# Kernel tuning notes

Measured on AMD Instinct MI355X. Metric: run time of the kernel, lower is better.

Reference implementation:

```python
import jax, jax.numpy as jnp
import numpy as np

PRUNE_N, PRUNE_M = 2, 4
RIA_A = 1.0
NUM_HEADS = 16
HEAD_DIM = 128
ROPE_THETA = 10000.0


def sparse_mask(W, scaler_row, perm):
    # RIA metric: |W|/colsum + |W|/rowsum, scaled by sqrt(scaler_row)**a
    absW = jnp.abs(W)
    metric = (absW / absW.sum(axis=0, keepdims=True)
              + absW / absW.sum(axis=1, keepdims=True))
    metric = metric * (jnp.sqrt(scaler_row)[None, :] ** RIA_A)
    Wm = metric @ perm                      # permute columns: [R, C]
    R, C = Wm.shape
    nb = C // PRUNE_M
    blocks = Wm.reshape(R, nb, PRUNE_M)
    # hard N:M mask: top-n per block of m
    _, idx = jax.lax.top_k(blocks, PRUNE_N)           # [R, nb, n]
    hard = jax.nn.one_hot(idx, PRUNE_M, dtype=Wm.dtype).sum(axis=-2)  # [R, nb, m]
    soft = jax.nn.softmax(blocks, axis=-1)
    hard = hard.reshape(R, C) @ perm.T
    soft = soft.reshape(R, C) @ perm.T
    # straight-through estimator
    return jax.lax.stop_gradient(hard - soft) + soft


def sparse_linear(x, W, b, scaler_row, perm):
    Wm = W * sparse_mask(W, scaler_row, perm)
    y = jnp.einsum('bsh,oh->bso', x, Wm)
    return y + b if b is not None else y


def rotate_half(x):
    x1, x2 = jnp.split(x, 2, axis=-1)
    return jnp.concatenate([-x2, x1], axis=-1)


def rope_tables(seq_len, dim, dtype):
    inv_freq = 1.0 / (ROPE_THETA ** (jnp.arange(0, dim, 2, dtype=jnp.float32) / dim))
    t = jnp.arange(seq_len, dtype=jnp.float32)
    freqs = jnp.outer(t, inv_freq)               # [S, dim/2]
    emb = jnp.concatenate([freqs, freqs], axis=-1)  # [S, dim]
    return jnp.cos(emb).astype(dtype), jnp.sin(emb).astype(dtype)


def setup_inputs() -> dict:
    key = jax.random.key(0)
    ks = jax.random.split(key, 16)
    H = 2048
    B, S = 2, 2048
    inp = {
        'hidden_states': jax.random.normal(ks[0], (B, S, H), jnp.float32) * 0.02,
        'Wq': jax.random.normal(ks[1], (H, H), jnp.float32) * 0.02,
        'bq': jax.random.normal(ks[2], (H,), jnp.float32) * 0.02,
        'Wk': jax.random.normal(ks[3], (H, H), jnp.float32) * 0.02,
        'bk': jax.random.normal(ks[4], (H,), jnp.float32) * 0.02,
        'Wv': jax.random.normal(ks[5], (H, H), jnp.float32) * 0.02,
        'bv': jax.random.normal(ks[6], (H,), jnp.float32) * 0.02,
        'Wo': jax.random.normal(ks[7], (H, H), jnp.float32) * 0.02,
        'sq': jax.random.uniform(ks[8], (H,), jnp.float32, 0.1, 1.0),
        'sk': jax.random.uniform(ks[9], (H,), jnp.float32, 0.1, 1.0),
        'sv': jax.random.uniform(ks[10], (H,), jnp.float32, 0.1, 1.0),
        'so': jax.random.uniform(ks[11], (H,), jnp.float32, 0.1, 1.0),
        'perm_qkv': jax.random.normal(ks[12], (H, H), jnp.float32) * 0.02,
        'perm_o': jax.random.normal(ks[13], (H, H), jnp.float32) * 0.02,
        'position_ids': jnp.broadcast_to(jnp.arange(S, dtype=jnp.int64), (B, S)),
    }
    return inp


def reference(hidden_states, Wq, bq, Wk, bk, Wv, bv, Wo,
              sq, sk, sv, so, perm_qkv, perm_o, position_ids):
    B, S, H = hidden_states.shape
    q = sparse_linear(hidden_states, Wq, bq, sq, perm_qkv)
    k = sparse_linear(hidden_states, Wk, bk, sk, perm_qkv)
    v = sparse_linear(hidden_states, Wv, bv, sv, perm_qkv)

    q = q.reshape(B, S, NUM_HEADS, HEAD_DIM).transpose(0, 2, 1, 3)  # [B,Hh,S,D]
    k = k.reshape(B, S, NUM_HEADS, HEAD_DIM).transpose(0, 2, 1, 3)
    v = v.reshape(B, S, NUM_HEADS, HEAD_DIM).transpose(0, 2, 1, 3)

    cos, sin = rope_tables(S, HEAD_DIM, q.dtype)
    c = cos[position_ids][:, None]  # [B,1,S,D]
    s = sin[position_ids][:, None]
    q = q * c + rotate_half(q) * s
    k = k * c + rotate_half(k) * s

    scores = jnp.einsum('bhqd,bhkd->bhqk', q, k) / np.sqrt(HEAD_DIM)
    causal = jnp.tril(jnp.ones((S, S), dtype=bool))
    scores = jnp.where(causal[None, None], scores, jnp.finfo(jnp.float32).min)
    attn = jax.nn.softmax(scores.astype(jnp.float32), axis=-1).astype(q.dtype)
    out = jnp.einsum('bhqk,bhkd->bhqd', attn, v)
    out = out.transpose(0, 2, 1, 3).reshape(B, S, H)
    out = sparse_linear(out, Wo, None, so, perm_o)
    return out
```

## Files before the change

### kernel.cpp

```cpp
#include <hip/hip_runtime.h>
#include <cstdint>
#include <cstddef>

typedef __attribute__((ext_vector_type(4))) float  f32x4;
typedef __attribute__((ext_vector_type(4))) int    i32x4;
typedef __attribute__((ext_vector_type(8))) short  s16x8;
typedef __attribute__((ext_vector_type(4))) short  s16x4;
typedef __attribute__((ext_vector_type(8))) __bf16 bf16x8;

struct Ptr4 { const float* p[4]; };

#define DEV __device__ __forceinline__

DEV unsigned short f2bf_u(float x) {
  unsigned u = __builtin_bit_cast(unsigned, x);
  u += 0x7fffu + ((u >> 16) & 1u);
  return (unsigned short)(u >> 16);
}
DEV float bfu2f(unsigned short u) {
  return __builtin_bit_cast(float, ((unsigned)u) << 16);
}
DEV bf16x8 ld_frag(const unsigned short* p) {
  s16x8 v = *(const s16x8*)p;
  return __builtin_bit_cast(bf16x8, v);
}
DEV f32x4 mfma16(bf16x8 a, bf16x8 b, f32x4 c) {
  return __builtin_amdgcn_mfma_f32_16x16x32_bf16(a, b, c, 0, 0, 0);
}
DEV void gload_lds16(const unsigned short* g, unsigned short* l) {
  __builtin_amdgcn_global_load_lds(
      (const __attribute__((address_space(1))) unsigned int*)g,
      (__attribute__((address_space(3))) unsigned int*)l, 16, 0, 0);
}
DEV int xcd_swizzle(int bid, int nwg) {
  const int q8 = nwg >> 3;
  return (bid & 7) * q8 + (bid >> 3);
}

__global__ __launch_bounds__(256)
void k_rowsum(Ptr4 Ws, float* __restrict__ rowsums)
{
  const int row = blockIdx.x, mat = blockIdx.y, tid = threadIdx.x;
  const float* W = Ws.p[mat] + (size_t)row * 2048;
  float s = 0.f;
  #pragma unroll
  for (int p = 0; p < 2; ++p) {
    f32x4 v = *(const f32x4*)(W + p * 1024 + tid * 4);
    s += fabsf(v[0]) + fabsf(v[1]) + fabsf(v[2]) + fabsf(v[3]);
  }
  #pragma unroll
  for (int off = 1; off < 64; off <<= 1) s += __shfl_xor(s, off);
  __shared__ float red[4];
  if ((tid & 63) == 0) red[tid >> 6] = s;
  __syncthreads();
  if (tid == 0) rowsums[mat * 2048 + row] = red[0] + red[1] + red[2] + red[3];
}

__global__ __launch_bounds__(256)
void k_colsum_part(Ptr4 Ws, float* __restrict__ part)
{
  const int c = blockIdx.x * 256 + threadIdx.x;
  const int r0 = blockIdx.y * 64;
  const int mat = blockIdx.z;
  const float* W = Ws.p[mat];
  float s = 0.f;
  for (int rr = 0; rr < 64; ++rr) s += fabsf(W[(size_t)(r0 + rr) * 2048 + c]);
  part[((size_t)mat * 32 + blockIdx.y) * 2048 + c] = s;
}
__global__ __launch_bounds__(256)
void k_colsum_red(const float* __restrict__ part, float* __restrict__ colsums)
{
  const int gid = blockIdx.x * 256 + threadIdx.x;
  const int mat = gid >> 11, c = gid & 2047;
  float s = 0.f;
  #pragma unroll
  for (int j = 0; j < 32; ++j) s += part[((size_t)mat * 32 + j) * 2048 + c];
  colsums[gid] = s;
}

__global__ __launch_bounds__(256)
void k_metric(Ptr4 Ws, Ptr4 Ss, const float* __restrict__ rowsums,
              const float* __restrict__ colsums,
              unsigned short* __restrict__ mhi, unsigned short* __restrict__ mlo)
{
  const size_t idx4 = ((size_t)blockIdx.x * 256 + threadIdx.x) * 4;
  const int row = (int)(idx4 >> 11);
  const int c = (int)(idx4 & 2047);
  const int mat = row >> 11, rl = row & 2047;
  const float rs = rowsums[mat * 2048 + rl];
  f32x4 w  = *(const f32x4*)(Ws.p[mat] + (size_t)rl * 2048 + c);
  f32x4 cs = *(const f32x4*)(colsums + mat * 2048 + c);
  f32x4 sv = *(const f32x4*)(Ss.p[mat] + c);
  s16x4 hv, lv;
  #pragma unroll
  for (int j = 0; j < 4; ++j) {
    const float a = fabsf(w[j]);
    const float m = (a / cs[j] + a / rs) * sqrtf(sv[j]);
    const unsigned short hb = f2bf_u(m);
    hv[j] = (short)hb;
    lv[j] = (short)f2bf_u(m - bfu2f(hb));
  }
  *(s16x4*)(mhi + idx4) = hv;
  *(s16x4*)(mlo + idx4) = lv;
}

__global__ __launch_bounds__(256)
void k_perm_prep(const float* __restrict__ pq, const float* __restrict__ po,
                 unsigned short* __restrict__ thi_q, unsigned short* __restrict__ tlo_q,
                 unsigned short* __restrict__ thi_o, unsigned short* __restrict__ tlo_o,
                 unsigned short* __restrict__ pb_q, unsigned short* __restrict__ pb_o)
{
  __shared__ float T[64 * 65];
  const int which = blockIdx.z;
  const float* src = which ? po : pq;
  unsigned short* thi = which ? thi_o : thi_q;
  unsigned short* tlo = which ? tlo_o : tlo_q;
  unsigned short* pb  = which ? pb_o : pb_q;
  const int rb = blockIdx.y * 64, cb = blockIdx.x * 64, tid = threadIdx.x;
  #pragma unroll
  for (int i = 0; i < 4; ++i) {
    const int cc = i * 256 + tid;
    const int rowl = cc >> 4, c4 = (cc & 15) * 4;
    f32x4 v = *(const f32x4*)(src + (size_t)(rb + rowl) * 2048 + cb + c4);
    s16x4 pc;
    #pragma unroll
    for (int j = 0; j < 4; ++j) {
      T[rowl * 65 + c4 + j] = v[j];
      pc[j] = (short)f2bf_u(v[j]);
    }
    *(s16x4*)(pb + (size_t)(rb + rowl) * 2048 + cb + c4) = pc;
  }
  __syncthreads();
  #pragma unroll
  for (int i = 0; i < 4; ++i) {
    const int cc = i * 256 + tid;
    const int rowt = cc >> 4, c4 = (cc & 15) * 4;
    s16x4 hh, ll;
    #pragma unroll
    for (int j = 0; j < 4; ++j) {
      const float v = T[(c4 + j) * 65 + rowt];
      const unsigned short hb = f2bf_u(v);
      hh[j] = (short)hb;
      ll[j] = (short)f2bf_u(v - bfu2f(hb));
    }
    const size_t off = (size_t)(cb + rowt) * 2048 + rb + c4;
    *(s16x4*)(thi + off) = hh;
    *(s16x4*)(tlo + off) = ll;
  }
}

__global__ __launch_bounds__(256)
void k_cast_bf(const float* __restrict__ src, unsigned short* __restrict__ dst)
{
  const size_t i = ((size_t)blockIdx.x * 256 + threadIdx.x) * 8;
  f32x4 a = *(const f32x4*)(src + i);
  f32x4 b = *(const f32x4*)(src + i + 4);
  s16x8 o;
  #pragma unroll
  for (int j = 0; j < 4; ++j) o[j] = (short)f2bf_u(a[j]);
  #pragma unroll
  for (int j = 0; j < 4; ++j) o[4 + j] = (short)f2bf_u(b[j]);
  *(s16x8*)(dst + i) = o;
}

__global__ __launch_bounds__(256)
void k_rope_tab(float* __restrict__ ct, float* __restrict__ st)
{
  const int gid = blockIdx.x * 256 + threadIdx.x;
  const int s = gid >> 6, i = gid & 63;
  const float ex = (float)(2 * i) / 128.f;
  const float inv = 1.f / powf(10000.f, ex);
  const float f = (float)s * inv;
  ct[gid] = cosf(f);
  st[gid] = sinf(f);
}

__global__ __launch_bounds__(256)
void k_rope_reshape(const unsigned short* __restrict__ yqkv, const int* __restrict__ pos,
                    const float* __restrict__ ct, const float* __restrict__ st,
                    unsigned short* __restrict__ qo, unsigned short* __restrict__ ko)
{
  const int gid = blockIdx.x * 256 + threadIdx.x;
  const int d8 = gid & 15;
  const int s = (gid >> 4) & 2047;
  const int h = (gid >> 15) & 15;
  const int b = gid >> 19;
  const int t = b * 2048 + s;
  const int p = pos[t];
  const size_t yb = (size_t)t * 6144 + h * 128;
  s16x8 qv = *(const s16x8*)(yqkv + yb + d8 * 8);
  s16x8 qp = *(const s16x8*)(yqkv + yb + (d8 ^ 8) * 8);
  s16x8 kv = *(const s16x8*)(yqkv + yb + 2048 + d8 * 8);
  s16x8 kp = *(const s16x8*)(yqkv + yb + 2048 + (d8 ^ 8) * 8);
  const int dh0 = (d8 & 7) * 8;
  const float sgn = (d8 < 8) ? -1.f : 1.f;
  s16x8 qo8, ko8;
  #pragma unroll
  for (int j = 0; j < 8; ++j) {
    const float cv = ct[p * 64 + dh0 + j];
    const float sv = st[p * 64 + dh0 + j];
    const float q0 = bfu2f((unsigned short)qv[j]);
    const float k0 = bfu2f((unsigned short)kv[j]);
    const float q1 = sgn * bfu2f((unsigned short)qp[j]);
    const float k1 = sgn * bfu2f((unsigned short)kp[j]);
    qo8[j] = (short)f2bf_u(q0 * cv + q1 * sv);
    ko8[j] = (short)f2bf_u(k0 * cv + k1 * sv);
  }
  const size_t o = ((size_t)(b * 16 + h) * 2048 + s) * 128 + d8 * 8;
  *(s16x8*)(qo + o) = qo8;
  *(s16x8*)(ko + o) = ko8;
}

__global__ __launch_bounds__(256)
void k_vtrans(const unsigned short* __restrict__ yqkv, unsigned short* __restrict__ vt)
{
  __shared__ float T[64 * 129];
  const int st = blockIdx.x, bh = blockIdx.y, tid = threadIdx.x;
  const int b = bh >> 4, h = bh & 15;
  #pragma unroll
  for (int i = 0; i < 4; ++i) {
    const int c = i * 256 + tid;
    const int sl = c >> 4, d8 = (c & 15) * 8;
    s16x8 v = *(const s16x8*)(yqkv + (size_t)(b * 2048 + st * 64 + sl) * 6144 + 4096 + h * 128 + d8);
    #pragma unroll
    for (int j = 0; j < 8; ++j) T[sl * 129 + d8 + j] = bfu2f((unsigned short)v[j]);
  }
  __syncthreads();
  #pragma unroll
  for (int i = 0; i < 4; ++i) {
    const int c = i * 256 + tid;
    const int d = c >> 3, s8 = (c & 7) * 8;
    s16x8 o;
    #pragma unroll
    for (int j = 0; j < 8; ++j) o[j] = (short)f2bf_u(T[(s8 + j) * 129 + d]);
    *(s16x8*)(vt + ((size_t)bh * 128 + d) * 2048 + st * 64 + s8) = o;
  }
}

template<int MODE, int SPLIT>
__global__ __launch_bounds__(256)
void gemm_bt(const unsigned short* __restrict__ Ahi, const unsigned short* __restrict__ Alo,
             const unsigned short* __restrict__ Bhi_1, const unsigned short* __restrict__ Blo_1,
             const unsigned short* __restrict__ Bhi_2, const unsigned short* __restrict__ Blo_2,
             int bswitch,
             float* __restrict__ Cf, unsigned short* __restrict__ Cb,
             Ptr4 aux, int M, int N, int K)
{
  __shared__ alignas(16) unsigned short As[2 * 4096];
  __shared__ alignas(16) unsigned short Bs[2 * 4096];
  const int tid = threadIdx.x;
  const int lane = tid & 63, wid = tid >> 6;
  const int wm = wid >> 1, wn = wid & 1;
  const int r = lane & 15, g = lane >> 4;
  const int nwg = gridDim.x * gridDim.y;
  const int sw = xcd_swizzle(blockIdx.y * gridDim.x + blockIdx.x, nwg);
  const int tx = sw % gridDim.x, ty = sw / gridDim.x;
  const int mbase = ty * 128;
  const int nbase = tx * 128;
  const int KT = K >> 5;
  (void)M;
  const unsigned short* Bhi = (mbase >= bswitch) ? Bhi_2 : Bhi_1;
  const unsigned short* Blo = (mbase >= bswitch) ? Blo_2 : Blo_1;

  const f32x4 zero = {0.f, 0.f, 0.f, 0.f};
  f32x4 acc[4][4];
  #pragma unroll
  for (int i = 0; i < 4; ++i) {
    #pragma unroll
    for (int j = 0; j < 4; ++j) acc[i][j] = zero;
  }

  const int srl = lane >> 2;
  const int sch = lane & 3;

  auto issue_tile = [&](int kt, int buf) {
    const size_t kb = (size_t)kt * 32;
    #pragma unroll
    for (int i = 0; i < 2; ++i) {
      const int rbase = wid * 32 + i * 16;
      const int rloc = rbase + srl;
      const int sc = ((sch ^ ((rloc >> 1) & 3)) << 3);
      const size_t ga = (size_t)(mbase + rloc) * K + kb + sc;
      const size_t gb = (size_t)(nbase + rloc) * K + kb + sc;
      gload_lds16(Ahi + ga, &As[buf * 4096 + rbase * 32]);
      gload_lds16(Bhi + gb, &Bs[buf * 4096 + rbase * 32]);
      if (SPLIT) {
        gload_lds16(Alo + ga, &As[4096 + rbase * 32]);
        gload_lds16(Blo + gb, &Bs[4096 + rbase * 32]);
      }
    }
  };

  if (SPLIT) {
    issue_tile(0, 0);
    for (int kt = 0; kt < KT; ++kt) {
      __syncthreads();

      bf16x8 ah[4], bfr[4], al[4], bl[4];
      #pragma unroll
      for (int mi = 0; mi < 4; ++mi) {
        const int arow = wm * 64 + mi * 16 + r;
        const int sw2 = ((g ^ ((arow >> 1) & 3)) << 3);
        ah[mi] = ld_frag(&As[arow * 32 + sw2]);
        al[mi] = ld_frag(&As[4096 + arow * 32 + sw2]);
      }
      #pragma unroll
      for (int ni = 0; ni < 4; ++ni) {
        const int brow = wn * 64 + ni * 16 + r;
        const int sw2 = ((g ^ ((brow >> 1) & 3)) << 3);
        bfr[ni] = ld_frag(&Bs[brow * 32 + sw2]);
        bl[ni] = ld_frag(&Bs[4096 + brow * 32 + sw2]);
      }
      __syncthreads();
      if (kt + 1 < KT) issue_tile(kt + 1, 0);

      #pragma unroll
      for (int mi = 0; mi < 4; ++mi) {
        #pragma unroll
        for (int ni = 0; ni < 4; ++ni) {
          acc[mi][ni] = mfma16(al[mi], bfr[ni], acc[mi][ni]);
          acc[mi][ni] = mfma16(ah[mi], bl[ni], acc[mi][ni]);
          acc[mi][ni] = mfma16(ah[mi], bfr[ni], acc[mi][ni]);
        }
      }
    }
  } else {
    issue_tile(0, 0);
    int cur = 0;
    for (int kt = 0; kt < KT; ++kt) {
      __syncthreads();
      if (kt + 1 < KT) issue_tile(kt + 1, cur ^ 1);

      bf16x8 ah[4], bfr[4];
      #pragma unroll
      for (int mi = 0; mi < 4; ++mi) {
        const int arow = wm * 64 + mi * 16 + r;
        ah[mi] = ld_frag(&As[cur * 4096 + arow * 32 + ((g ^ ((arow >> 1) & 3)) << 3)]);
      }
      #pragma unroll
      for (int ni = 0; ni < 4; ++ni) {
        const int brow = wn * 64 + ni * 16 + r;
        bfr[ni] = ld_frag(&Bs[cur * 4096 + brow * 32 + ((g ^ ((brow >> 1) & 3)) << 3)]);
      }
      #pragma unroll
      for (int mi = 0; mi < 4; ++mi) {
        #pragma unroll
        for (int ni = 0; ni < 4; ++ni)
          acc[mi][ni] = mfma16(ah[mi], bfr[ni], acc[mi][ni]);
      }
      cur ^= 1;
    }
  }

  #pragma unroll
  for (int mi = 0; mi < 4; ++mi) {
    #pragma unroll
    for (int ni = 0; ni < 4; ++ni) {
      const int row0 = mbase + wm * 64 + mi * 16 + g * 4;
      const int col  = nbase + wn * 64 + ni * 16 + r;
      if (MODE == 0) {
        #pragma unroll
        for (int e = 0; e < 4; ++e)
          Cf[(size_t)(row0 + e) * N + col] = acc[mi][ni][e];
      } else if (MODE == 1) {
        const float* wsrc = aux.p[row0 >> 11];
        #pragma unroll
        for (int e = 0; e < 4; ++e) {
          const float mval = wsrc[(size_t)((row0 + e) & 2047) * 2048 + col];
          Cb[(size_t)(row0 + e) * N + col] = f2bf_u(acc[mi][ni][e] * mval);
        }
      } else if (MODE == 2) {
        const float* bp = aux.p[col >> 11];
        const float bb = bp[col & 2047];
        #pragma unroll
        for (int e = 0; e < 4; ++e)
          Cb[(size_t)(row0 + e) * N + col] = f2bf_u(acc[mi][ni][e] + bb);
      } else {
        const int ii = r & 3;
        #pragma unroll
        for (int e = 0; e < 4; ++e) {
          const float v  = acc[mi][ni][e];
          const float v1 = __shfl_xor(v, 1);
          const float v2 = __shfl_xor(v, 2);
          const float v3 = __shfl_xor(v, 3);
          int cnt = 0;
          { const int j = ii ^ 1; cnt += (v1 > v) || (v1 == v && j < ii); }
          { const int j = ii ^ 2; cnt += (v2 > v) || (v2 == v && j < ii); }
          { const int j = ii ^ 3; cnt += (v3 > v) || (v3 == v && j < ii); }
          Cb[(size_t)(row0 + e) * N + col] =
              (cnt < 2) ? (unsigned short)0x3F80 : (unsigned short)0;
        }
      }
    }
  }
}

__global__ __launch_bounds__(256)
void attn_fa(const unsigned short* __restrict__ Qh, const unsigned short* __restrict__ Kh,
             const unsigned short* __restrict__ Vt, unsigned short* __restrict__ Out)
{
  __shared__ alignas(16) unsigned short Ks[64 * 128];
  __shared__ alignas(16) unsigned short Vs[128 * 64];
  __shared__ alignas(16) unsigned short Ps[4][1024];
  const int tid = threadIdx.x, lane = tid & 63, wid = tid >> 6;
  const int r = lane & 15, g = lane >> 4;
  const int sw = xcd_swizzle(blockIdx.y * gridDim.x + blockIdx.x, gridDim.x * gridDim.y);
  const int pair = sw % 16, bh = sw / 16;
  const int b = bh >> 4, h = bh & 15;
  const f32x4 zero = {0.f, 0.f, 0.f, 0.f};

  i32x4 kr[4], vr[4];
  auto issue_kv = [&](int kvt) {
    #pragma unroll
    for (int i = 0; i < 4; ++i) {
      const int c = i * 256 + tid;
      {
        const int row = c >> 4, slot = c & 15;
        kr[i] = *(const i32x4*)(Kh + ((size_t)bh * 2048 + kvt * 64 + row) * 128 + slot * 8);
      }
      {
        const int row = c >> 3, slot = c & 7;
        vr[i] = *(const i32x4*)(Vt + ((size_t)bh * 128 + row) * 2048 + kvt * 64 + slot * 8);
      }
    }
  };

  for (int half = 0; half < 2; ++half) {
    const int qt = half ? (31 - pair) : pair;
    const int qrow0 = qt * 64 + wid * 16;

    bf16x8 qf[4];
    {
      const unsigned short* qp = Qh + ((size_t)bh * 2048 + qrow0 + r) * 128;
      #pragma unroll
      for (int ks = 0; ks < 4; ++ks) qf[ks] = ld_frag(qp + ks * 32 + g * 8);
    }
    f32x4 oacc[8];
    #pragma unroll
    for (int i = 0; i < 8; ++i) oacc[i] = zero;
    float m_run[4] = {-1e30f, -1e30f, -1e30f, -1e30f};
    float l_run[4] = {0.f, 0.f, 0.f, 0.f};

    issue_kv(0);
    for (int kvt = 0; kvt <= qt; ++kvt) {
      __syncthreads();
      #pragma unroll
      for (int i = 0; i < 4; ++i) {
        const int c = i * 256 + tid;
        {
          const int row = c >> 4, slot = c & 15;
          *(i32x4*)&Ks[row * 128 + ((slot ^ (row & 7)) << 3)] = kr[i];
        }
        {
          const int row = c >> 3, slot = c & 7;
          *(i32x4*)&Vs[row * 64 + ((slot ^ (row & 7)) << 3)] = vr[i];
        }
      }
      __syncthreads();
      if (kvt < qt) issue_kv(kvt + 1);

      f32x4 sc[4];
      #pragma unroll
      for (int ni = 0; ni < 4; ++ni) sc[ni] = zero;
      __builtin_amdgcn_s_setprio(1);
      #pragma unroll
      for (int ks = 0; ks < 4; ++ks) {
        const int slot = (ks << 2) | g;
        #pragma unroll
        for (int ni = 0; ni < 4; ++ni) {
          const int krow = ni * 16 + r;
          bf16x8 kf = ld_frag(&Ks[krow * 128 + ((slot ^ (krow & 7)) << 3)]);
          sc[ni] = mfma16(qf[ks], kf, sc[ni]);
        }
      }
      __builtin_amdgcn_s_setprio(0);
      const float sscale = 0.08838834764831845f;
      if (kvt == qt) {
        #pragma unroll
        for (int ni = 0; ni < 4; ++ni) {
          const int kvg = kvt * 64 + ni * 16 + r;
          #pragma unroll
          for (int e = 0; e < 4; ++e) {
            const int qg = qrow0 + g * 4 + e;
            const float s = sc[ni][e] * sscale;
            sc[ni][e] = (kvg > qg) ? -1e30f : s;
          }
        }
      } else {
        #pragma unroll
        for (int ni = 0; ni < 4; ++ni) {
          #pragma unroll
          for (int e = 0; e < 4; ++e) sc[ni][e] *= sscale;
        }
      }
      float corr[4];
      #pragma unroll
      for (int e = 0; e < 4; ++e) {
        float mx = fmaxf(fmaxf(sc[0][e], sc[1][e]), fmaxf(sc[2][e], sc[3][e]));
        mx = fmaxf(mx, __shfl_xor(mx, 1));
        mx = fmaxf(mx, __shfl_xor(mx, 2));
        mx = fmaxf(mx, __shfl_xor(mx, 4));
        mx = fmaxf(mx, __shfl_xor(mx, 8));
        const float mn = fmaxf(m_run[e], mx);
        corr[e] = exp2f((m_run[e] - mn) * 1.4426950408889634f);
        m_run[e] = mn;
      }
      float psum[4] = {0.f, 0.f, 0.f, 0.f};
      #pragma unroll
      for (int ni = 0; ni < 4; ++ni) {
        #pragma unroll
        for (int e = 0; e < 4; ++e) {
          const float p = exp2f((sc[ni][e] - m_run[e]) * 1.4426950408889634f);
          sc[ni][e] = p;
          psum[e] += p;
        }
      }
      #pragma unroll
      for (int e = 0; e < 4; ++e) {
        float s = psum[e];
        s += __shfl_xor(s, 1);
        s += __shfl_xor(s, 2);
        s += __shfl_xor(s, 4);
        s += __shfl_xor(s, 8);
        l_run[e] = l_run[e] * corr[e] + s;
      }
      #pragma unroll
      for (int nf = 0; nf < 8; ++nf) {
        #pragma unroll
        for (int e = 0; e < 4; ++e) oacc[nf][e] *= corr[e];
      }
      #pragma unroll
      for (int ni = 0; ni < 4; ++ni) {
        #pragma unroll
        for (int e = 0; e < 4; ++e) {
          const int prow = g * 4 + e;
          const int col = ni * 16 + r;
          const int slot = col >> 3;
          Ps[wid][prow * 64 + ((slot ^ (prow & 7)) << 3) + (col & 7)] = f2bf_u(sc[ni][e]);
        }
      }
      __builtin_amdgcn_s_setprio(1);
      #pragma unroll
      for (int ks = 0; ks < 2; ++ks) {
        const int slot = (ks << 2) | g;
        bf16x8 pf = ld_frag(&Ps[wid][r * 64 + ((slot ^ (r & 7)) << 3)]);
        #pragma unroll
        for (int nf = 0; nf < 8; ++nf) {
          const int vrow = nf * 16 + r;
          bf16x8 vf = ld_frag(&Vs[vrow * 64 + ((slot ^ (vrow & 7)) << 3)]);
          oacc[nf] = mfma16(pf, vf, oacc[nf]);
        }
      }
      __builtin_amdgcn_s_setprio(0);
    }
    #pragma unroll
    for (int e = 0; e < 4; ++e) {
      const float inv = 1.f / l_run[e];
      const int qg = qrow0 + g * 4 + e;
      #pragma unroll
      for (int nf = 0; nf < 8; ++nf) {
        const int d = nf * 16 + r;
        Out[((size_t)(b * 2048 + qg)) * 2048 + h * 128 + d] = f2bf_u(oacc[nf][e] * inv);
      }
    }
  }
}

extern "C" void kernel_launch(void* const* d_in, const int* in_sizes, int n_in,
                              void* d_out, int out_size, void* d_ws, size_t ws_size,
                              hipStream_t stream)
{
  (void)in_sizes; (void)n_in; (void)out_size; (void)ws_size;
  const float* hid   = (const float*)d_in[0];
  const float* Wq    = (const float*)d_in[1];
  const float* bq    = (const float*)d_in[2];
  const float* Wk    = (const float*)d_in[3];
  const float* bk    = (const float*)d_in[4];
  const float* Wv    = (const float*)d_in[5];
  const float* bv    = (const float*)d_in[6];
  const float* Wo    = (const float*)d_in[7];
  const float* sq    = (const float*)d_in[8];
  const float* sk    = (const float*)d_in[9];
  const float* sv    = (const float*)d_in[10];
  const float* so    = (const float*)d_in[11];
  const float* permq = (const float*)d_in[12];
  const float* permo = (const float*)d_in[13];
  const int* pos     = (const int*)d_in[14];
  float* out = (float*)d_out;
  char* ws = (char*)d_ws;

  constexpr size_t OFF_ROWS = 0;
  constexpr size_t OFF_COLS = OFF_ROWS + (size_t)4 * 2048 * 4;
  constexpr size_t OFF_PART = OFF_COLS + (size_t)4 * 2048 * 4;
  constexpr size_t OFF_COS  = OFF_PART + (size_t)4 * 32 * 2048 * 4;
  constexpr size_t OFF_SIN  = OFF_COS + (size_t)2048 * 64 * 4;
  constexpr size_t SZ_PERM  = (size_t)2048 * 2048 * 2;
  constexpr size_t OFF_A    = OFF_SIN + (size_t)2048 * 64 * 4;
  constexpr size_t OFF_PTQH = OFF_A;
  constexpr size_t OFF_PTQL = OFF_PTQH + SZ_PERM;
  constexpr size_t OFF_PTOH = OFF_PTQL + SZ_PERM;
  constexpr size_t OFF_PTOL = OFF_PTOH + SZ_PERM;
  constexpr size_t OFF_PBQ  = OFF_PTOL + SZ_PERM;
  constexpr size_t OFF_PBO  = OFF_PBQ + SZ_PERM;
  constexpr size_t SZ_M8    = (size_t)8192 * 2048 * 2;
  constexpr size_t OFF_B    = OFF_PBO + SZ_PERM;
  constexpr size_t OFF_C    = OFF_B + SZ_M8;
  constexpr size_t OFF_D    = OFF_C + SZ_M8;
  constexpr size_t OFF_E    = OFF_D + SZ_M8;

  float* rowsums = (float*)(ws + OFF_ROWS);
  float* colsums = (float*)(ws + OFF_COLS);
  float* part    = (float*)(ws + OFF_PART);
  float* cost    = (float*)(ws + OFF_COS);
  float* sint    = (float*)(ws + OFF_SIN);
  unsigned short* ptqh = (unsigned short*)(ws + OFF_PTQH);
  unsigned short* ptql = (unsigned short*)(ws + OFF_PTQL);
  unsigned short* ptoh = (unsigned short*)(ws + OFF_PTOH);
  unsigned short* ptol = (unsigned short*)(ws + OFF_PTOL);
  unsigned short* pbq  = (unsigned short*)(ws + OFF_PBQ);
  unsigned short* pbo  = (unsigned short*)(ws + OFF_PBO);
  unsigned short* mhi  = (unsigned short*)(ws + OFF_B);
  unsigned short* mlo  = (unsigned short*)(ws + OFF_C);
  unsigned short* hard = (unsigned short*)(ws + OFF_D);
  unsigned short* wfin = (unsigned short*)(ws + OFF_E);
  unsigned short* yqkv = (unsigned short*)(ws + OFF_B);
  unsigned short* qhb  = (unsigned short*)(ws + OFF_A);
  unsigned short* khb  = (unsigned short*)(ws + OFF_A + 2 * SZ_PERM);
  unsigned short* vtg  = (unsigned short*)(ws + OFF_A + 4 * SZ_PERM);
  unsigned short* xbf  = (unsigned short*)(ws + OFF_D);
  unsigned short* att  = (unsigned short*)(ws + OFF_D + SZ_M8 / 2);

  Ptr4 Wptrs{{Wq, Wk, Wv, Wo}};
  Ptr4 Sptrs{{sq, sk, sv, so}};
  Ptr4 BiasP{{bq, bk, bv, nullptr}};
  Ptr4 NoAux{{nullptr, nullptr, nullptr, nullptr}};
  constexpr int NOSW = 1 << 30;

  k_rowsum<<<dim3(2048, 4), 256, 0, stream>>>(Wptrs, rowsums);
  k_colsum_part<<<dim3(8, 32, 4), 256, 0, stream>>>(Wptrs, part);
  k_colsum_red<<<32, 256, 0, stream>>>(part, colsums);
  k_metric<<<16384, 256, 0, stream>>>(Wptrs, Sptrs, rowsums, colsums, mhi, mlo);
  k_perm_prep<<<dim3(32, 32, 2), 256, 0, stream>>>(permq, permo, ptqh, ptql, ptoh, ptol, pbq, pbo);
  gemm_bt<3, 1><<<dim3(16, 64), 256, 0, stream>>>(mhi, mlo, ptqh, ptql, ptoh, ptol, 6144,
                                                  nullptr, hard, NoAux, 8192, 2048, 2048);
  gemm_bt<1, 0><<<dim3(16, 64), 256, 0, stream>>>(hard, nullptr, pbq, nullptr, pbo, nullptr, 6144,
                                                  nullptr, wfin, Wptrs, 8192, 2048, 2048);
  k_cast_bf<<<4096, 256, 0, stream>>>(hid, xbf);
  gemm_bt<2, 0><<<dim3(48, 32), 256, 0, stream>>>(xbf, nullptr, wfin, nullptr, wfin, nullptr, NOSW,
                                                  nullptr, yqkv, BiasP, 4096, 6144, 2048);
  k_rope_tab<<<512, 256, 0, stream>>>(cost, sint);
  k_rope_reshape<<<4096, 256, 0, stream>>>(yqkv, pos, cost, sint, qhb, khb);
  k_vtrans<<<dim3(32, 32), 256, 0, stream>>>(yqkv, vtg);
  attn_fa<<<dim3(16, 32), 256, 0, stream>>>(qhb, khb, vtg, att);
  gemm_bt<0, 0><<<dim3(16, 32), 256, 0, stream>>>(att, nullptr, wfin + (size_t)6144 * 2048, nullptr,
                                                  wfin + (size_t)6144 * 2048, nullptr, NOSW,
                                                  out, nullptr, NoAux, 4096, 2048, 2048);
}
```

Baseline: 649.8 us.

## Double-buffer split-precision GEMM tiles and drop XCD workgroup swizzle

The split (hi/lo bf16) GEMM path now allocates double-buffered LDS for both hi and lo tiles. It prefetches the next k-tile right after the barrier, so each iteration needs one __syncthreads instead of two and global loads overlap with the three MFMAs. The change also removes the XCD swizzle of block indices in favor of plain blockIdx mapping, which may reduce L2 locality. LDS use for the SPLIT variant doubles to 64 KB per block, which can lower occupancy.

```diff
diff --git a/kernel.cpp b/kernel.cpp
--- a/kernel.cpp
+++ b/kernel.cpp
@@ -246,17 +246,15 @@
              float* __restrict__ Cf, unsigned short* __restrict__ Cb,
              Ptr4 aux, int M, int N, int K)
 {
-  __shared__ alignas(16) unsigned short As[2 * 4096];
-  __shared__ alignas(16) unsigned short Bs[2 * 4096];
+  constexpr int LO = 2 * 4096;
+  __shared__ alignas(16) unsigned short As[(SPLIT ? 4 : 2) * 4096];
+  __shared__ alignas(16) unsigned short Bs[(SPLIT ? 4 : 2) * 4096];
   const int tid = threadIdx.x;
   const int lane = tid & 63, wid = tid >> 6;
   const int wm = wid >> 1, wn = wid & 1;
   const int r = lane & 15, g = lane >> 4;
-  const int nwg = gridDim.x * gridDim.y;
-  const int sw = xcd_swizzle(blockIdx.y * gridDim.x + blockIdx.x, nwg);
-  const int tx = sw % gridDim.x, ty = sw / gridDim.x;
-  const int mbase = ty * 128;
-  const int nbase = tx * 128;
+  const int mbase = blockIdx.y * 128;
+  const int nbase = blockIdx.x * 128;
   const int KT = K >> 5;
   (void)M;
   const unsigned short* Bhi = (mbase >= bswitch) ? Bhi_2 : Bhi_1;
@@ -285,35 +283,41 @@
       gload_lds16(Ahi + ga, &As[buf * 4096 + rbase * 32]);
       gload_lds16(Bhi + gb, &Bs[buf * 4096 + rbase * 32]);
       if (SPLIT) {
-        gload_lds16(Alo + ga, &As[4096 + rbase * 32]);
-        gload_lds16(Blo + gb, &Bs[4096 + rbase * 32]);
+        gload_lds16(Alo + ga, &As[LO + buf * 4096 + rbase * 32]);
+        gload_lds16(Blo + gb, &Bs[LO + buf * 4096 + rbase * 32]);
       }
     }
   };
 
-  if (SPLIT) {
-    issue_tile(0, 0);
-    for (int kt = 0; kt < KT; ++kt) {
-      __syncthreads();
-
-      bf16x8 ah[4], bfr[4], al[4], bl[4];
+  issue_tile(0, 0);
+  int cur = 0;
+  for (int kt = 0; kt < KT; ++kt) {
+    __syncthreads();
+    if (kt + 1 < KT) issue_tile(kt + 1, cur ^ 1);
+
+    bf16x8 ah[4], bfr[4];
+    #pragma unroll
+    for (int mi = 0; mi < 4; ++mi) {
+      const int arow = wm * 64 + mi * 16 + r;
+      ah[mi] = ld_frag(&As[cur * 4096 + arow * 32 + ((g ^ ((arow >> 1) & 3)) << 3)]);
+    }
+    #pragma unroll
+    for (int ni = 0; ni < 4; ++ni) {
+      const int brow = wn * 64 + ni * 16 + r;
+      bfr[ni] = ld_frag(&Bs[cur * 4096 + brow * 32 + ((g ^ ((brow >> 1) & 3)) << 3)]);
+    }
+    if (SPLIT) {
+      bf16x8 al[4], bl[4];
       #pragma unroll
       for (int mi = 0; mi < 4; ++mi) {
         const int arow = wm * 64 + mi * 16 + r;
-        const int sw2 = ((g ^ ((arow >> 1) & 3)) << 3);
-        ah[mi] = ld_frag(&As[arow * 32 + sw2]);
-        al[mi] = ld_frag(&As[4096 + arow * 32 + sw2]);
+        al[mi] = ld_frag(&As[LO + cur * 4096 + arow * 32 + ((g ^ ((arow >> 1) & 3)) << 3)]);
       }
       #pragma unroll
       for (int ni = 0; ni < 4; ++ni) {
         const int brow = wn * 64 + ni * 16 + r;
-        const int sw2 = ((g ^ ((brow >> 1) & 3)) << 3);
-        bfr[ni] = ld_frag(&Bs[brow * 32 + sw2]);
-        bl[ni] = ld_frag(&Bs[4096 + brow * 32 + sw2]);
-      }
-      __syncthreads();
-      if (kt + 1 < KT) issue_tile(kt + 1, 0);
-
+        bl[ni] = ld_frag(&Bs[LO + cur * 4096 + brow * 32 + ((g ^ ((brow >> 1) & 3)) << 3)]);
+      }
       #pragma unroll
       for (int mi = 0; mi < 4; ++mi) {
         #pragma unroll
@@ -323,33 +327,15 @@
           acc[mi][ni] = mfma16(ah[mi], bfr[ni], acc[mi][ni]);
         }
       }
-    }
-  } else {
-    issue_tile(0, 0);
-    int cur = 0;
-    for (int kt = 0; kt < KT; ++kt) {
-      __syncthreads();
-      if (kt + 1 < KT) issue_tile(kt + 1, cur ^ 1);
-
-      bf16x8 ah[4], bfr[4];
-      #pragma unroll
-      for (int mi = 0; mi < 4; ++mi) {
-        const int arow = wm * 64 + mi * 16 + r;
-        ah[mi] = ld_frag(&As[cur * 4096 + arow * 32 + ((g ^ ((arow >> 1) & 3)) << 3)]);
-      }
-      #pragma unroll
-      for (int ni = 0; ni < 4; ++ni) {
-        const int brow = wn * 64 + ni * 16 + r;
-        bfr[ni] = ld_frag(&Bs[cur * 4096 + brow * 32 + ((g ^ ((brow >> 1) & 3)) << 3)]);
-      }
+    } else {
       #pragma unroll
       for (int mi = 0; mi < 4; ++mi) {
         #pragma unroll
         for (int ni = 0; ni < 4; ++ni)
           acc[mi][ni] = mfma16(ah[mi], bfr[ni], acc[mi][ni]);
       }
-      cur ^= 1;
-    }
+    }
+    cur ^= 1;
   }
 
   #pragma unroll
```

New measurement: 659.2 us. No clear change (+1.4%).
